# Kernel tuning notes

Measured on AMD Instinct MI355X. Metric: run time of the kernel, lower is better.

The kernel has to match this reference:

```python
import jax, jax.numpy as jnp
import numpy as np

N, L, E, H = 256, 128, 1024, 16
D = E // H
S = 2  # len(stride_tokens_index); must satisfy S*L == N for the final reshape


def setup_inputs() -> dict:
    key = jax.random.key(0)
    ks = jax.random.split(key, 10)
    s = 1.0 / np.sqrt(E)
    return {
        "values": jax.random.normal(ks[0], (N, L, E), jnp.float32),
        "keys": jax.random.normal(ks[1], (N, L, E), jnp.float32),
        "query": jax.random.normal(ks[2], (N, L, E), jnp.float32),
        "mask": jnp.ones((L, L), jnp.float32),
        "Wv": jax.random.normal(ks[3], (E, E), jnp.float32) * s,
        "bv": jnp.zeros((E,), jnp.float32),
        "Wk": jax.random.normal(ks[4], (E, E), jnp.float32) * s,
        "bk": jnp.zeros((E,), jnp.float32),
        "Wq": jax.random.normal(ks[5], (E, E), jnp.float32) * s,
        "bq": jnp.zeros((E,), jnp.float32),
        "Wo": jax.random.normal(ks[6], (E, E), jnp.float32) * s,
        "bo": jnp.zeros((E,), jnp.float32),
        "token_index": 3,
        "stride_tokens_index": jnp.sort(jax.random.randint(ks[7], (S,), 0, N)),
    }


def reference(values, keys, query, mask, Wv, bv, Wk, bk, Wq, bq, Wo, bo,
              token_index, stride_tokens_index):
    # Linear projections (torch nn.Linear: x @ W.T + b), then split heads
    v = (values @ Wv.T + bv).reshape(N, L, H, D)
    k = (keys @ Wk.T + bk).reshape(N, L, H, D)
    q = (query @ Wq.T + bq).reshape(N, L, H, D)
    # queries[[token_index]] -> (1, L, H, D); we drop the singleton and broadcast
    q_sel = q[token_index]              # (L, H, D)
    k_sel = k[stride_tokens_index]      # (S, L, H, D)
    v_sel = v[stride_tokens_index]      # (S, L, H, D)
    # einsum('nqhd,nkhd->nhqk') with broadcast n=1 vs n=S
    energy = jnp.einsum('qhd,nkhd->nhqk', q_sel, k_sel)   # (S, H, L, L)
    energy = jnp.where(mask == 0, jnp.float32(-1e20), energy)
    attn = jax.nn.softmax(energy / jnp.sqrt(jnp.float32(E)), axis=3)
    wv = jnp.einsum('nhql,nlhd->nqhd', attn, v_sel)        # (S, L, H, D)
    # reshape(N, 1, E) relies on S*L == N (as in the original module)
    out = wv.reshape(N, 1, E) @ Wo.T + bo
    return out.squeeze(1)                                   # (N, E)
```

## Files before the change

### kernel.cpp

```cpp
#include <hip/hip_runtime.h>


#define LL 128
#define EE 1024
#define HH 16
#define DD 64
#define SS 2

typedef unsigned short u16;
typedef unsigned int   u32;
typedef __attribute__((ext_vector_type(8))) short short8;
typedef __attribute__((ext_vector_type(4))) float floatx4;

__device__ inline u32 pack_trunc(float lo, float hi) {
    return (__float_as_uint(hi) & 0xFFFF0000u) | (__float_as_uint(lo) >> 16);
}
__device__ inline u16 f2bf_rne(float f) {
    u32 u = __float_as_uint(f);
    return (u16)((u + 0x7FFFu + ((u >> 16) & 1u)) >> 16);
}
__device__ inline float bf2f(u16 x) { return __uint_as_float(((u32)x) << 16); }

__device__ inline short8 frag_from_f32(const float* __restrict__ p) {
    floatx4 a = *(const floatx4*)p;
    floatx4 b = *(const floatx4*)(p + 4);
    union { short8 s; u32 w[4]; } r;
    r.w[0] = pack_trunc(a[0], a[1]);
    r.w[1] = pack_trunc(a[2], a[3]);
    r.w[2] = pack_trunc(b[0], b[1]);
    r.w[3] = pack_trunc(b[2], b[3]);
    return r.s;
}

__device__ inline int clamp_idx(int v) {
    return ((unsigned)v < 256u) ? v : (v & 255);
}

__global__ __launch_bounds__(64) void proj_mfma(
    const float* __restrict__ values, const float* __restrict__ keys,
    const float* __restrict__ query,
    const float* __restrict__ Wv, const float* __restrict__ bv,
    const float* __restrict__ Wk, const float* __restrict__ bk,
    const float* __restrict__ Wq, const float* __restrict__ bq,
    const int* __restrict__ tok, const int* __restrict__ sidx,
    u16* __restrict__ q_sel, u16* __restrict__ k_sel, u16* __restrict__ v_sel)
{
    const size_t LE = (size_t)LL * EE;
    const int job = blockIdx.z;
    const float *src, *W, *bias;
    u16* dst;
    if (job == 0)      { src = query  + (size_t)clamp_idx(tok[0])  * LE;
                         W = Wq; bias = bq; dst = q_sel; }
    else if (job <= 2) { const int s = job - 1;
                         src = keys   + (size_t)clamp_idx(sidx[s]) * LE;
                         W = Wk; bias = bk; dst = k_sel + s * LE; }
    else               { const int s = job - 3;
                         src = values + (size_t)clamp_idx(sidx[s]) * LE;
                         W = Wv; bias = bv; dst = v_sel + s * LE; }

    const int lane = threadIdx.x;
    const int lm   = lane & 15, kq = (lane >> 4) * 8;
    const int row0 = blockIdx.x * 32, col0 = blockIdx.y * 32;

    floatx4 acc[2][2] = {};
    const float* a0p = src + (size_t)(row0 + lm) * EE + kq;
    const float* a1p = a0p + 16 * EE;
    const float* b0p = W   + (size_t)(col0 + lm) * EE + kq;
    const float* b1p = b0p + 16 * EE;

    short8 a0 = frag_from_f32(a0p), a1 = frag_from_f32(a1p);
    short8 b0 = frag_from_f32(b0p), b1 = frag_from_f32(b1p);
    for (int k0 = 32; k0 < EE; k0 += 32) {
        short8 na0 = frag_from_f32(a0p + k0);
        short8 na1 = frag_from_f32(a1p + k0);
        short8 nb0 = frag_from_f32(b0p + k0);
        short8 nb1 = frag_from_f32(b1p + k0);
        acc[0][0] = __builtin_amdgcn_mfma_f32_16x16x32_bf16(a0, b0, acc[0][0], 0, 0, 0);
        acc[0][1] = __builtin_amdgcn_mfma_f32_16x16x32_bf16(a0, b1, acc[0][1], 0, 0, 0);
        acc[1][0] = __builtin_amdgcn_mfma_f32_16x16x32_bf16(a1, b0, acc[1][0], 0, 0, 0);
        acc[1][1] = __builtin_amdgcn_mfma_f32_16x16x32_bf16(a1, b1, acc[1][1], 0, 0, 0);
        a0 = na0; a1 = na1; b0 = nb0; b1 = nb1;
    }
    acc[0][0] = __builtin_amdgcn_mfma_f32_16x16x32_bf16(a0, b0, acc[0][0], 0, 0, 0);
    acc[0][1] = __builtin_amdgcn_mfma_f32_16x16x32_bf16(a0, b1, acc[0][1], 0, 0, 0);
    acc[1][0] = __builtin_amdgcn_mfma_f32_16x16x32_bf16(a1, b0, acc[1][0], 0, 0, 0);
    acc[1][1] = __builtin_amdgcn_mfma_f32_16x16x32_bf16(a1, b1, acc[1][1], 0, 0, 0);

    const int rbase = (lane >> 4) * 4;
    #pragma unroll
    for (int i = 0; i < 2; ++i)
        #pragma unroll
        for (int j = 0; j < 2; ++j) {
            const int ccol = col0 + j * 16 + lm;
            const float bb = bias[ccol];
            #pragma unroll
            for (int r = 0; r < 4; ++r) {
                const int crow = row0 + i * 16 + rbase + r;
                dst[(size_t)crow * EE + ccol] = f2bf_rne(acc[i][j][r] + bb);
            }
        }
}

__global__ __launch_bounds__(64) void attn_simple(
    const u16* __restrict__ q_sel,
    const u16* __restrict__ k_sel,
    const u16* __restrict__ v_sel,
    const float* __restrict__ mask,
    u16* __restrict__ wv)
{
    __shared__ float p[LL];
    const int lane = threadIdx.x;
    const int q = blockIdx.x, h = blockIdx.y, s = blockIdx.z;

    const u16* Qr = q_sel + (size_t)q * EE + h * DD;
    const u16* K0 = k_sel + ((size_t)s * LL + lane) * EE + h * DD;
    const u16* K1 = K0 + (size_t)64 * EE;

    float e0 = 0.f, e1 = 0.f;
    #pragma unroll
    for (int d = 0; d < DD; ++d) {
        const float qv = bf2f(Qr[d]);
        e0 += qv * bf2f(K0[d]);
        e1 += qv * bf2f(K1[d]);
    }

    const float scale = 1.0f / 32.0f;
    const float m0 = mask[q * LL + lane];
    const float m1 = mask[q * LL + lane + 64];
    e0 = (m0 == 0.f ? -1.0e20f : e0) * scale;
    e1 = (m1 == 0.f ? -1.0e20f : e1) * scale;

    float m = fmaxf(e0, e1);
    #pragma unroll
    for (int off = 32; off >= 1; off >>= 1) m = fmaxf(m, __shfl_xor(m, off));
    const float p0 = __expf(e0 - m), p1 = __expf(e1 - m);
    float sum = p0 + p1;
    #pragma unroll
    for (int off = 32; off >= 1; off >>= 1) sum += __shfl_xor(sum, off);
    const float inv = 1.0f / sum;
    p[lane]      = p0 * inv;
    p[lane + 64] = p1 * inv;
    __syncthreads();

    const u16* Vb = v_sel + (size_t)s * LL * EE + h * DD + lane;
    float acc = 0.f;
    for (int k = 0; k < LL; ++k)
        acc += p[k] * bf2f(Vb[(size_t)k * EE]);
    wv[((size_t)s * LL + q) * EE + h * DD + lane] = f2bf_rne(acc);
}

__global__ __launch_bounds__(64) void outproj_mfma(
    const u16* __restrict__ wv, const float* __restrict__ Wo,
    const float* __restrict__ bo, float* __restrict__ out)
{
    const int lane = threadIdx.x;
    const int lm   = lane & 15, kq = (lane >> 4) * 8;
    const int row0 = blockIdx.x * 32, col0 = blockIdx.y * 32;

    floatx4 acc[2][2] = {};
    const u16*   a0p = wv + (size_t)(row0 + lm) * EE + kq;
    const u16*   a1p = a0p + 16 * EE;
    const float* b0p = Wo + (size_t)(col0 + lm) * EE + kq;
    const float* b1p = b0p + 16 * EE;

    short8 a0 = *(const short8*)a0p;
    short8 a1 = *(const short8*)a1p;
    short8 b0 = frag_from_f32(b0p);
    short8 b1 = frag_from_f32(b1p);
    for (int k0 = 32; k0 < EE; k0 += 32) {
        short8 na0 = *(const short8*)(a0p + k0);
        short8 na1 = *(const short8*)(a1p + k0);
        short8 nb0 = frag_from_f32(b0p + k0);
        short8 nb1 = frag_from_f32(b1p + k0);
        acc[0][0] = __builtin_amdgcn_mfma_f32_16x16x32_bf16(a0, b0, acc[0][0], 0, 0, 0);
        acc[0][1] = __builtin_amdgcn_mfma_f32_16x16x32_bf16(a0, b1, acc[0][1], 0, 0, 0);
        acc[1][0] = __builtin_amdgcn_mfma_f32_16x16x32_bf16(a1, b0, acc[1][0], 0, 0, 0);
        acc[1][1] = __builtin_amdgcn_mfma_f32_16x16x32_bf16(a1, b1, acc[1][1], 0, 0, 0);
        a0 = na0; a1 = na1; b0 = nb0; b1 = nb1;
    }
    acc[0][0] = __builtin_amdgcn_mfma_f32_16x16x32_bf16(a0, b0, acc[0][0], 0, 0, 0);
    acc[0][1] = __builtin_amdgcn_mfma_f32_16x16x32_bf16(a0, b1, acc[0][1], 0, 0, 0);
    acc[1][0] = __builtin_amdgcn_mfma_f32_16x16x32_bf16(a1, b0, acc[1][0], 0, 0, 0);
    acc[1][1] = __builtin_amdgcn_mfma_f32_16x16x32_bf16(a1, b1, acc[1][1], 0, 0, 0);

    const int rbase = (lane >> 4) * 4;
    #pragma unroll
    for (int i = 0; i < 2; ++i)
        #pragma unroll
        for (int j = 0; j < 2; ++j) {
            const int ccol = col0 + j * 16 + lm;
            const float bb = bo[ccol];
            #pragma unroll
            for (int r = 0; r < 4; ++r) {
                const int crow = row0 + i * 16 + rbase + r;
                out[(size_t)crow * EE + ccol] = acc[i][j][r] + bb;
            }
        }
}

extern "C" void kernel_launch(void* const* d_in, const int* in_sizes, int n_in,
                              void* d_out, int out_size, void* d_ws, size_t ws_size,
                              hipStream_t stream) {
    const float* values = (const float*)d_in[0];
    const float* keys   = (const float*)d_in[1];
    const float* query  = (const float*)d_in[2];
    const float* mask   = (const float*)d_in[3];
    const float* Wv     = (const float*)d_in[4];
    const float* bv     = (const float*)d_in[5];
    const float* Wk     = (const float*)d_in[6];
    const float* bk     = (const float*)d_in[7];
    const float* Wq     = (const float*)d_in[8];
    const float* bq     = (const float*)d_in[9];
    const float* Wo     = (const float*)d_in[10];
    const float* bo     = (const float*)d_in[11];
    const int*   tok    = (const int*)d_in[12];
    const int*   sidx   = (const int*)d_in[13];
    float* out = (float*)d_out;

    const size_t LE = (size_t)LL * EE;
    u16* q_sel = (u16*)d_ws;
    u16* k_sel = q_sel + LE;
    u16* v_sel = k_sel + SS * LE;
    u16* wv    = v_sel + SS * LE;

    proj_mfma<<<dim3(4, 32, 5), 64, 0, stream>>>(
        values, keys, query, Wv, bv, Wk, bk, Wq, bq, tok, sidx,
        q_sel, k_sel, v_sel);

    attn_simple<<<dim3(128, 16, 2), 64, 0, stream>>>(
        q_sel, k_sel, v_sel, mask, wv);

    outproj_mfma<<<dim3(8, 32, 1), 64, 0, stream>>>(
        wv, Wo, bo, out);
}
```

Measured before the change: 359.7 us.

## Fuse projection, attention and output projection into one persistent kernel with grid barriers

Replaces the three kernel launches with a single persistent kernel of 256 blocks of 4 waves. Blocks are separated by atomic-counter grid barriers, and the barrier counter is cleared by a memset before each launch. The goal is to remove launch gaps and the tail of each stage. The attention stage is also reworked: each wave handles 4 queries, uses vectorized Q/K loads, and broadcasts probabilities with shuffles instead of LDS. The output projection moves to 16x16 tiles so the work is spread over 1024 waves. The grid barrier relies on all blocks being co-resident, and the smaller output tiles lose some operand reuse.

```diff
diff --git a/kernel.cpp b/kernel.cpp
--- a/kernel.cpp
+++ b/kernel.cpp
@@ -6,6 +6,7 @@
 #define HH 16
 #define DD 64
 #define SS 2
+#define NBLK 256
 
 typedef unsigned short u16;
 typedef unsigned int   u32;
@@ -36,166 +37,176 @@
     return ((unsigned)v < 256u) ? v : (v & 255);
 }
 
-__global__ __launch_bounds__(64) void proj_mfma(
+__device__ inline void grid_sync(u32* bar, u32 target) {
+    __syncthreads();
+    if (threadIdx.x == 0) {
+        __threadfence();
+        atomicAdd(bar, 1u);
+        while (atomicAdd(bar, 0u) < target)
+            __builtin_amdgcn_s_sleep(8);
+        __threadfence();
+    }
+    __syncthreads();
+}
+
+__global__ __launch_bounds__(256) void fused_attn(
     const float* __restrict__ values, const float* __restrict__ keys,
-    const float* __restrict__ query,
+    const float* __restrict__ query,  const float* __restrict__ mask,
     const float* __restrict__ Wv, const float* __restrict__ bv,
     const float* __restrict__ Wk, const float* __restrict__ bk,
     const float* __restrict__ Wq, const float* __restrict__ bq,
+    const float* __restrict__ Wo, const float* __restrict__ bo,
     const int* __restrict__ tok, const int* __restrict__ sidx,
-    u16* __restrict__ q_sel, u16* __restrict__ k_sel, u16* __restrict__ v_sel)
+    u16* __restrict__ q_sel, u16* __restrict__ k_sel, u16* __restrict__ v_sel,
+    u16* __restrict__ wv, u32* __restrict__ bar, float* __restrict__ out)
 {
+    const int tid  = threadIdx.x;
+    const int lane = tid & 63;
+    const int w    = tid >> 6;
+    const int b    = blockIdx.x;
+    const int gid  = b * 4 + w;
     const size_t LE = (size_t)LL * EE;
-    const int job = blockIdx.z;
-    const float *src, *W, *bias;
-    u16* dst;
-    if (job == 0)      { src = query  + (size_t)clamp_idx(tok[0])  * LE;
-                         W = Wq; bias = bq; dst = q_sel; }
-    else if (job <= 2) { const int s = job - 1;
-                         src = keys   + (size_t)clamp_idx(sidx[s]) * LE;
-                         W = Wk; bias = bk; dst = k_sel + s * LE; }
-    else               { const int s = job - 3;
-                         src = values + (size_t)clamp_idx(sidx[s]) * LE;
-                         W = Wv; bias = bv; dst = v_sel + s * LE; }
-
-    const int lane = threadIdx.x;
-    const int lm   = lane & 15, kq = (lane >> 4) * 8;
-    const int row0 = blockIdx.x * 32, col0 = blockIdx.y * 32;
-
-    floatx4 acc[2][2] = {};
-    const float* a0p = src + (size_t)(row0 + lm) * EE + kq;
-    const float* a1p = a0p + 16 * EE;
-    const float* b0p = W   + (size_t)(col0 + lm) * EE + kq;
-    const float* b1p = b0p + 16 * EE;
-
-    short8 a0 = frag_from_f32(a0p), a1 = frag_from_f32(a1p);
-    short8 b0 = frag_from_f32(b0p), b1 = frag_from_f32(b1p);
-    for (int k0 = 32; k0 < EE; k0 += 32) {
-        short8 na0 = frag_from_f32(a0p + k0);
-        short8 na1 = frag_from_f32(a1p + k0);
-        short8 nb0 = frag_from_f32(b0p + k0);
-        short8 nb1 = frag_from_f32(b1p + k0);
-        acc[0][0] = __builtin_amdgcn_mfma_f32_16x16x32_bf16(a0, b0, acc[0][0], 0, 0, 0);
-        acc[0][1] = __builtin_amdgcn_mfma_f32_16x16x32_bf16(a0, b1, acc[0][1], 0, 0, 0);
-        acc[1][0] = __builtin_amdgcn_mfma_f32_16x16x32_bf16(a1, b0, acc[1][0], 0, 0, 0);
-        acc[1][1] = __builtin_amdgcn_mfma_f32_16x16x32_bf16(a1, b1, acc[1][1], 0, 0, 0);
-        a0 = na0; a1 = na1; b0 = nb0; b1 = nb1;
-    }
-    acc[0][0] = __builtin_amdgcn_mfma_f32_16x16x32_bf16(a0, b0, acc[0][0], 0, 0, 0);
-    acc[0][1] = __builtin_amdgcn_mfma_f32_16x16x32_bf16(a0, b1, acc[0][1], 0, 0, 0);
-    acc[1][0] = __builtin_amdgcn_mfma_f32_16x16x32_bf16(a1, b0, acc[1][0], 0, 0, 0);
-    acc[1][1] = __builtin_amdgcn_mfma_f32_16x16x32_bf16(a1, b1, acc[1][1], 0, 0, 0);
-
-    const int rbase = (lane >> 4) * 4;
-    #pragma unroll
-    for (int i = 0; i < 2; ++i)
+
+    {
+        const int t = w * NBLK + b;
+        if (t < 640) {
+            const int job  = t >> 7;
+            const int rem  = t & 127;
+            const int row0 = (rem >> 5) * 32;
+            const int col0 = (rem & 31) * 32;
+            const float *src, *W, *bias; u16* dst;
+            if (job == 0)      { src = query  + (size_t)clamp_idx(tok[0])  * LE;
+                                 W = Wq; bias = bq; dst = q_sel; }
+            else if (job <= 2) { const int s = job - 1;
+                                 src = keys   + (size_t)clamp_idx(sidx[s]) * LE;
+                                 W = Wk; bias = bk; dst = k_sel + s * LE; }
+            else               { const int s = job - 3;
+                                 src = values + (size_t)clamp_idx(sidx[s]) * LE;
+                                 W = Wv; bias = bv; dst = v_sel + s * LE; }
+
+            const int lm = lane & 15, kq = (lane >> 4) * 8;
+            floatx4 acc[2][2] = {};
+            const float* a0p = src + (size_t)(row0 + lm) * EE + kq;
+            const float* a1p = a0p + 16 * EE;
+            const float* b0p = W   + (size_t)(col0 + lm) * EE + kq;
+            const float* b1p = b0p + 16 * EE;
+
+            short8 a0 = frag_from_f32(a0p), a1 = frag_from_f32(a1p);
+            short8 b0 = frag_from_f32(b0p), b1 = frag_from_f32(b1p);
+            for (int k0 = 32; k0 < EE; k0 += 32) {
+                short8 na0 = frag_from_f32(a0p + k0);
+                short8 na1 = frag_from_f32(a1p + k0);
+                short8 nb0 = frag_from_f32(b0p + k0);
+                short8 nb1 = frag_from_f32(b1p + k0);
+                acc[0][0] = __builtin_amdgcn_mfma_f32_16x16x32_bf16(a0, b0, acc[0][0], 0, 0, 0);
+                acc[0][1] = __builtin_amdgcn_mfma_f32_16x16x32_bf16(a0, b1, acc[0][1], 0, 0, 0);
+                acc[1][0] = __builtin_amdgcn_mfma_f32_16x16x32_bf16(a1, b0, acc[1][0], 0, 0, 0);
+                acc[1][1] = __builtin_amdgcn_mfma_f32_16x16x32_bf16(a1, b1, acc[1][1], 0, 0, 0);
+                a0 = na0; a1 = na1; b0 = nb0; b1 = nb1;
+            }
+            acc[0][0] = __builtin_amdgcn_mfma_f32_16x16x32_bf16(a0, b0, acc[0][0], 0, 0, 0);
+            acc[0][1] = __builtin_amdgcn_mfma_f32_16x16x32_bf16(a0, b1, acc[0][1], 0, 0, 0);
+            acc[1][0] = __builtin_amdgcn_mfma_f32_16x16x32_bf16(a1, b0, acc[1][0], 0, 0, 0);
+            acc[1][1] = __builtin_amdgcn_mfma_f32_16x16x32_bf16(a1, b1, acc[1][1], 0, 0, 0);
+
+            const int rbase = (lane >> 4) * 4;
+            #pragma unroll
+            for (int i = 0; i < 2; ++i)
+                #pragma unroll
+                for (int j = 0; j < 2; ++j) {
+                    const int ccol = col0 + j * 16 + lm;
+                    const float bb = bias[ccol];
+                    #pragma unroll
+                    for (int r = 0; r < 4; ++r) {
+                        const int crow = row0 + i * 16 + rbase + r;
+                        dst[(size_t)crow * EE + ccol] = f2bf_rne(acc[i][j][r] + bb);
+                    }
+                }
+        }
+    }
+
+    grid_sync(&bar[0], NBLK);
+
+    {
+        const int hs = gid >> 5;
+        const int s  = hs >> 4, h = hs & 15;
+        const int q0 = (gid & 31) * 4;
+        const u16* K0 = k_sel + ((size_t)s * LL + lane) * EE + h * DD;
+        const u16* K1 = K0 + (size_t)64 * EE;
+        const u16* Vb = v_sel + (size_t)s * LL * EE + h * DD + lane;
+        const float scale = 1.0f / 32.0f;
+
+        for (int i = 0; i < 4; ++i) {
+            const int q = q0 + i;
+            const u16* Qr = q_sel + (size_t)q * EE + h * DD;
+
+            float e0 = 0.f, e1 = 0.f;
+            #pragma unroll
+            for (int d8 = 0; d8 < 8; ++d8) {
+                short8 qv  = *(const short8*)(Qr + d8 * 8);
+                short8 k0v = *(const short8*)(K0 + d8 * 8);
+                short8 k1v = *(const short8*)(K1 + d8 * 8);
+                #pragma unroll
+                for (int j = 0; j < 8; ++j) {
+                    const float qf = bf2f((u16)qv[j]);
+                    e0 += qf * bf2f((u16)k0v[j]);
+                    e1 += qf * bf2f((u16)k1v[j]);
+                }
+            }
+
+            const float m0 = mask[q * LL + lane];
+            const float m1 = mask[q * LL + lane + 64];
+            e0 = (m0 == 0.f ? -1.0e20f : e0) * scale;
+            e1 = (m1 == 0.f ? -1.0e20f : e1) * scale;
+
+            float m = fmaxf(e0, e1);
+            #pragma unroll
+            for (int off = 32; off >= 1; off >>= 1) m = fmaxf(m, __shfl_xor(m, off));
+            float p0 = __expf(e0 - m), p1 = __expf(e1 - m);
+            float sum = p0 + p1;
+            #pragma unroll
+            for (int off = 32; off >= 1; off >>= 1) sum += __shfl_xor(sum, off);
+            const float inv = 1.0f / sum;
+            p0 *= inv; p1 *= inv;
+
+            float acc0 = 0.f, acc1 = 0.f;
+            #pragma unroll 8
+            for (int k = 0; k < 64; ++k) {
+                acc0 += __shfl(p0, k) * bf2f(Vb[(size_t)k * EE]);
+                acc1 += __shfl(p1, k) * bf2f(Vb[(size_t)(k + 64) * EE]);
+            }
+            wv[((size_t)s * LL + q) * EE + h * DD + lane] = f2bf_rne(acc0 + acc1);
+        }
+    }
+
+    grid_sync(&bar[1], NBLK);
+
+    {
+        const int row0 = (gid >> 6) * 16;
+        const int col0 = (gid & 63) * 16;
+        const int lm = lane & 15, kq = (lane >> 4) * 8;
+
+        floatx4 acc = {0.f, 0.f, 0.f, 0.f};
+        const u16*   ap = wv + (size_t)(row0 + lm) * EE + kq;
+        const float* bp = Wo + (size_t)(col0 + lm) * EE + kq;
+
+        short8 a = *(const short8*)ap;
+        short8 bf = frag_from_f32(bp);
+        for (int k0 = 32; k0 < EE; k0 += 32) {
+            short8 na = *(const short8*)(ap + k0);
+            short8 nb = frag_from_f32(bp + k0);
+            acc = __builtin_amdgcn_mfma_f32_16x16x32_bf16(a, bf, acc, 0, 0, 0);
+            a = na; bf = nb;
+        }
+        acc = __builtin_amdgcn_mfma_f32_16x16x32_bf16(a, bf, acc, 0, 0, 0);
+
+        const int rbase = (lane >> 4) * 4;
+        const int ccol  = col0 + lm;
+        const float bb  = bo[ccol];
         #pragma unroll
-        for (int j = 0; j < 2; ++j) {
-            const int ccol = col0 + j * 16 + lm;
-            const float bb = bias[ccol];
-            #pragma unroll
-            for (int r = 0; r < 4; ++r) {
-                const int crow = row0 + i * 16 + rbase + r;
-                dst[(size_t)crow * EE + ccol] = f2bf_rne(acc[i][j][r] + bb);
-            }
-        }
-}
-
-__global__ __launch_bounds__(64) void attn_simple(
-    const u16* __restrict__ q_sel,
-    const u16* __restrict__ k_sel,
-    const u16* __restrict__ v_sel,
-    const float* __restrict__ mask,
-    u16* __restrict__ wv)
-{
-    __shared__ float p[LL];
-    const int lane = threadIdx.x;
-    const int q = blockIdx.x, h = blockIdx.y, s = blockIdx.z;
-
-    const u16* Qr = q_sel + (size_t)q * EE + h * DD;
-    const u16* K0 = k_sel + ((size_t)s * LL + lane) * EE + h * DD;
-    const u16* K1 = K0 + (size_t)64 * EE;
-
-    float e0 = 0.f, e1 = 0.f;
-    #pragma unroll
-    for (int d = 0; d < DD; ++d) {
-        const float qv = bf2f(Qr[d]);
-        e0 += qv * bf2f(K0[d]);
-        e1 += qv * bf2f(K1[d]);
-    }
-
-    const float scale = 1.0f / 32.0f;
-    const float m0 = mask[q * LL + lane];
-    const float m1 = mask[q * LL + lane + 64];
-    e0 = (m0 == 0.f ? -1.0e20f : e0) * scale;
-    e1 = (m1 == 0.f ? -1.0e20f : e1) * scale;
-
-    float m = fmaxf(e0, e1);
-    #pragma unroll
-    for (int off = 32; off >= 1; off >>= 1) m = fmaxf(m, __shfl_xor(m, off));
-    const float p0 = __expf(e0 - m), p1 = __expf(e1 - m);
-    float sum = p0 + p1;
-    #pragma unroll
-    for (int off = 32; off >= 1; off >>= 1) sum += __shfl_xor(sum, off);
-    const float inv = 1.0f / sum;
-    p[lane]      = p0 * inv;
-    p[lane + 64] = p1 * inv;
-    __syncthreads();
-
-    const u16* Vb = v_sel + (size_t)s * LL * EE + h * DD + lane;
-    float acc = 0.f;
-    for (int k = 0; k < LL; ++k)
-        acc += p[k] * bf2f(Vb[(size_t)k * EE]);
-    wv[((size_t)s * LL + q) * EE + h * DD + lane] = f2bf_rne(acc);
-}
-
-__global__ __launch_bounds__(64) void outproj_mfma(
-    const u16* __restrict__ wv, const float* __restrict__ Wo,
-    const float* __restrict__ bo, float* __restrict__ out)
-{
-    const int lane = threadIdx.x;
-    const int lm   = lane & 15, kq = (lane >> 4) * 8;
-    const int row0 = blockIdx.x * 32, col0 = blockIdx.y * 32;
-
-    floatx4 acc[2][2] = {};
-    const u16*   a0p = wv + (size_t)(row0 + lm) * EE + kq;
-    const u16*   a1p = a0p + 16 * EE;
-    const float* b0p = Wo + (size_t)(col0 + lm) * EE + kq;
-    const float* b1p = b0p + 16 * EE;
-
-    short8 a0 = *(const short8*)a0p;
-    short8 a1 = *(const short8*)a1p;
-    short8 b0 = frag_from_f32(b0p);
-    short8 b1 = frag_from_f32(b1p);
-    for (int k0 = 32; k0 < EE; k0 += 32) {
-        short8 na0 = *(const short8*)(a0p + k0);
-        short8 na1 = *(const short8*)(a1p + k0);
-        short8 nb0 = frag_from_f32(b0p + k0);
-        short8 nb1 = frag_from_f32(b1p + k0);
-        acc[0][0] = __builtin_amdgcn_mfma_f32_16x16x32_bf16(a0, b0, acc[0][0], 0, 0, 0);
-        acc[0][1] = __builtin_amdgcn_mfma_f32_16x16x32_bf16(a0, b1, acc[0][1], 0, 0, 0);
-        acc[1][0] = __builtin_amdgcn_mfma_f32_16x16x32_bf16(a1, b0, acc[1][0], 0, 0, 0);
-        acc[1][1] = __builtin_amdgcn_mfma_f32_16x16x32_bf16(a1, b1, acc[1][1], 0, 0, 0);
-        a0 = na0; a1 = na1; b0 = nb0; b1 = nb1;
-    }
-    acc[0][0] = __builtin_amdgcn_mfma_f32_16x16x32_bf16(a0, b0, acc[0][0], 0, 0, 0);
-    acc[0][1] = __builtin_amdgcn_mfma_f32_16x16x32_bf16(a0, b1, acc[0][1], 0, 0, 0);
-    acc[1][0] = __builtin_amdgcn_mfma_f32_16x16x32_bf16(a1, b0, acc[1][0], 0, 0, 0);
-    acc[1][1] = __builtin_amdgcn_mfma_f32_16x16x32_bf16(a1, b1, acc[1][1], 0, 0, 0);
-
-    const int rbase = (lane >> 4) * 4;
-    #pragma unroll
-    for (int i = 0; i < 2; ++i)
-        #pragma unroll
-        for (int j = 0; j < 2; ++j) {
-            const int ccol = col0 + j * 16 + lm;
-            const float bb = bo[ccol];
-            #pragma unroll
-            for (int r = 0; r < 4; ++r) {
-                const int crow = row0 + i * 16 + rbase + r;
-                out[(size_t)crow * EE + ccol] = acc[i][j][r] + bb;
-            }
-        }
+        for (int r = 0; r < 4; ++r)
+            out[(size_t)(row0 + rbase + r) * EE + ccol] = acc[r] + bb;
+    }
 }
 
 extern "C" void kernel_launch(void* const* d_in, const int* in_sizes, int n_in,
@@ -222,14 +233,11 @@
     u16* k_sel = q_sel + LE;
     u16* v_sel = k_sel + SS * LE;
     u16* wv    = v_sel + SS * LE;
-
-    proj_mfma<<<dim3(4, 32, 5), 64, 0, stream>>>(
-        values, keys, query, Wv, bv, Wk, bk, Wq, bq, tok, sidx,
-        q_sel, k_sel, v_sel);
-
-    attn_simple<<<dim3(128, 16, 2), 64, 0, stream>>>(
-        q_sel, k_sel, v_sel, mask, wv);
-
-    outproj_mfma<<<dim3(8, 32, 1), 64, 0, stream>>>(
-        wv, Wo, bo, out);
-}
+    u32* bar   = (u32*)((char*)d_ws + (1792u * 1024u));
+
+    hipMemsetAsync(bar, 0, 64, stream);
+
+    fused_attn<<<dim3(NBLK), dim3(256), 0, stream>>>(
+        values, keys, query, mask, Wv, bv, Wk, bk, Wq, bq, Wo, bo,
+        tok, sidx, q_sel, k_sel, v_sel, wv, bar, out);
+}
```

Result: slower. 386.0 us (+7.3%).
